# Kernel tuning notes

Measured on AMD Instinct MI355X. Metric: run time of the kernel, lower is better.

## Reference

```python
import jax, jax.numpy as jnp
import numpy as np

B, DIM, N_SIDE = 32, 256, 32
HEADS, DIM_K, DIM_U = 4, 16, 1
DIM_V = 64  # dim_out // heads
EPS = 1e-5

def _rel_pos_idx(n):
    # matches calc_rel_pos: meshgrid(ij) -> (N,2), pairwise diff + (n-1)
    i = np.arange(n)
    pos = np.stack(np.meshgrid(i, i, indexing='ij'), 0).reshape(2, -1).T  # (N, 2)
    rel = pos[None, :] - pos[:, None] + (n - 1)                            # (N, N, 2)
    return rel[..., 0], rel[..., 1]

def _bn(t, gamma, beta):
    # BatchNorm2d in training mode: batch stats over (B, H, W), biased var
    mu = t.mean(axis=(0, 2, 3), keepdims=True)
    var = t.var(axis=(0, 2, 3), keepdims=True)
    xhat = (t - mu) * jax.lax.rsqrt(var + EPS)
    return xhat * gamma[None, :, None, None] + beta[None, :, None, None]

def setup_inputs() -> dict:
    key = jax.random.key(0)
    ks = jax.random.split(key, 5)
    rl = 2 * N_SIDE - 1
    return {
        'x': jax.random.normal(ks[0], (B, DIM, N_SIDE, N_SIDE), jnp.float32),
        'w_q': jax.random.normal(ks[1], (DIM_K * HEADS, DIM), jnp.float32) * 0.05,
        'w_k': jax.random.normal(ks[2], (DIM_K * DIM_U, DIM), jnp.float32) * 0.05,
        'w_v': jax.random.normal(ks[3], (DIM_V * DIM_U, DIM), jnp.float32) * 0.05,
        'gamma_q': jnp.ones((DIM_K * HEADS,), jnp.float32),
        'beta_q': jnp.zeros((DIM_K * HEADS,), jnp.float32),
        'gamma_v': jnp.ones((DIM_V * DIM_U,), jnp.float32),
        'beta_v': jnp.zeros((DIM_V * DIM_U,), jnp.float32),
        'rel_pos_emb': jax.random.normal(ks[4], (rl, rl, DIM_K, DIM_U), jnp.float32),
    }

def reference(x, w_q, w_k, w_v, gamma_q, beta_q, gamma_v, beta_v, rel_pos_emb):
    b, c, hh, ww = x.shape
    n = hh * ww
    # 1x1 convs as channel contractions
    q = _bn(jnp.einsum('oc,bchw->bohw', w_q, x), gamma_q, beta_q)
    k = jnp.einsum('oc,bchw->bohw', w_k, x)
    v = _bn(jnp.einsum('oc,bchw->bohw', w_v, x), gamma_v, beta_v)
    q = q.reshape(b, HEADS, DIM_K, n)   # b h k n
    k = k.reshape(b, DIM_U, DIM_K, n)   # b u k m
    v = v.reshape(b, DIM_U, DIM_V, n)   # b u v m
    k = jax.nn.softmax(k, axis=-1)
    # content lambda
    lam_c = jnp.einsum('bukm,buvm->bkv', k, v)
    Yc = jnp.einsum('bhkn,bkv->bhvn', q, lam_c)
    # positional lambda via relative-position embedding gather
    ni, mi = _rel_pos_idx(N_SIDE)
    emb = rel_pos_emb[ni, mi]                      # (n, n, k, u)
    lam_p = jnp.einsum('nmku,buvm->bnkv', emb, v)  # dominant compute
    Yp = jnp.einsum('bhkn,bnkv->bhvn', q, lam_p)
    Y = Yc + Yp                                    # b h v n
    return Y.reshape(b, HEADS * DIM_V, hh, ww)
```

## Files before the change

kernel.cpp:

```cpp
#include <hip/hip_runtime.h>

using u16 = unsigned short;
using u32 = unsigned int;

typedef __attribute__((ext_vector_type(4))) float f32x4;
typedef __attribute__((ext_vector_type(4))) u16 u16x4;
typedef __attribute__((ext_vector_type(8))) u16 u16x8;
typedef __attribute__((ext_vector_type(8))) short s16x8;

__device__ __forceinline__ u16 f2bf(float f) {
  u32 x = __builtin_bit_cast(u32, f);
  x += 0x7fffu + ((x >> 16) & 1u);
  return (u16)(x >> 16);
}
__device__ __forceinline__ float bf2f(u16 u) {
  u32 x = ((u32)u) << 16;
  return __builtin_bit_cast(float, x);
}

__device__ __forceinline__ void glds16(const u16* gsrc, u16* ldst) {
  __builtin_amdgcn_global_load_lds(
      (const __attribute__((address_space(1))) unsigned int*)gsrc,
      (__attribute__((address_space(3))) unsigned int*)ldst, 16, 0, 0);
}

__global__ __launch_bounds__(256) void k_prep(
    const float* __restrict__ wq, const float* __restrict__ wk,
    const float* __restrict__ wv, const float* __restrict__ R,
    u16* __restrict__ Wb, u16* __restrict__ APre)
{
  const int blk = blockIdx.x;
  const int t = threadIdx.x;
  if (blk < 144) {
    const int o = blk;
    const float* src = (o < 64) ? (wq + o * 256)
                     : (o < 80) ? (wk + (o - 64) * 256)
                                : (wv + (o - 80) * 256);
    Wb[o * 256 + t] = f2bf(src[t]);
  } else {
    const int di = blk - 144;
    const int w = t >> 6, l = t & 63;
    const int g = l >> 4, k = l & 15;
    for (int j1 = w; j1 < 32; j1 += 4) {
      u16x8 o8;
#pragma unroll
      for (int e = 0; e < 8; ++e) {
        int dj = 8 * g + e - j1 + 31;
        o8[e] = f2bf(R[(di * 63 + dj) * 16 + k]);
      }
      *(u16x8*)(APre + ((di * 32 + j1) * 64 + l) * 8) = o8;
    }
  }
}

union ProjSmem {
  u16 XLb[64][264];
  float SS[2][160];
};

__global__ __launch_bounds__(256) void k_proj(
    const float* __restrict__ x, const u16* __restrict__ Wb,
    float* __restrict__ q_raw, float* __restrict__ k_raw,
    float* __restrict__ v_raw,
    float* __restrict__ qs1, float* __restrict__ qs2,
    float* __restrict__ vs1, float* __restrict__ vs2)
{
  __shared__ ProjSmem PS;
  const int b  = blockIdx.x >> 4;
  const int p0 = (blockIdx.x & 15) * 64;
  const int t  = threadIdx.x;

  {
    const int p4 = (t & 15) * 4;
    const int cb = (t >> 4);
#pragma unroll
    for (int i = 0; i < 8; ++i) {
      const int c = 2 * (i * 16 + cb);
      f32x4 xa = *(const f32x4*)&x[(b * 256 + c) * 1024 + p0 + p4];
      f32x4 xb = *(const f32x4*)&x[(b * 256 + c + 1) * 1024 + p0 + p4];
#pragma unroll
      for (int j = 0; j < 4; ++j) {
        u32 pk = (u32)f2bf(xa[j]) | ((u32)f2bf(xb[j]) << 16);
        *(u32*)&PS.XLb[p4 + j][c] = pk;
      }
    }
  }
  __syncthreads();

  const int w  = t >> 6;
  const int l  = t & 63;
  const int g  = l >> 4;
  const int cc = l & 15;
  const int p  = p0 + w * 16 + cc;

  f32x4 acc[9];
  const f32x4 fz = {0.f, 0.f, 0.f, 0.f};
#pragma unroll
  for (int mt = 0; mt < 9; ++mt) acc[mt] = fz;

#pragma unroll
  for (int ko = 0; ko < 8; ++ko) {
    s16x8 bfr = *(const s16x8*)&PS.XLb[w * 16 + cc][ko * 32 + g * 8];
#pragma unroll
    for (int mt = 0; mt < 9; ++mt) {
      s16x8 afr = *(const s16x8*)&Wb[(mt * 16 + cc) * 256 + ko * 32 + g * 8];
      acc[mt] = __builtin_amdgcn_mfma_f32_16x16x32_bf16(afr, bfr, acc[mt], 0, 0, 0);
    }
  }

#pragma unroll
  for (int mt = 0; mt < 9; ++mt) {
#pragma unroll
    for (int r = 0; r < 4; ++r) {
      const int o = mt * 16 + 4 * g + r;
      const float val = acc[mt][r];
      if (mt < 4)       q_raw[(b * 64 + o) * 1024 + p] = val;
      else if (mt == 4) k_raw[(b * 16 + (o - 64)) * 1024 + p] = val;
      else              v_raw[(b * 64 + (o - 80)) * 1024 + p] = val;
    }
  }

  __syncthreads();
  {
    float* ss = &PS.SS[0][0];
    for (int i = t; i < 320; i += 256) ss[i] = 0.f;
  }
  __syncthreads();
#pragma unroll
  for (int mt = 0; mt < 9; ++mt) {
    if (mt == 4) continue;
#pragma unroll
    for (int r = 0; r < 4; ++r) {
      float s1 = acc[mt][r];
      float s2 = s1 * s1;
#pragma unroll
      for (int off = 1; off < 16; off <<= 1) {
        s1 += __shfl_xor(s1, off);
        s2 += __shfl_xor(s2, off);
      }
      if (cc == 0) {
        const int o = mt * 16 + 4 * g + r;
        atomicAdd(&PS.SS[0][o], s1);
        atomicAdd(&PS.SS[1][o], s2);
      }
    }
  }
  __syncthreads();
  if (t < 64) {
    atomicAdd(&qs1[t], PS.SS[0][t]);
    atomicAdd(&qs2[t], PS.SS[1][t]);
  } else if (t >= 80 && t < 144) {
    atomicAdd(&vs1[t - 80], PS.SS[0][t]);
    atomicAdd(&vs2[t - 80], PS.SS[1][t]);
  }
}

__global__ __launch_bounds__(256) void k_soft(
    const float* __restrict__ k_raw,
    float* __restrict__ kmax, float* __restrict__ kinv)
{
  const int t = threadIdx.x;
  const int w = t >> 6, lane = t & 63;
  const int row = blockIdx.x * 4 + w;
  const f32x4* kr4 = (const f32x4*)(k_raw + row * 1024 + lane * 16);
  f32x4 a0 = kr4[0], a1 = kr4[1], a2 = kr4[2], a3 = kr4[3];
  float mx = -3.0e38f;
#pragma unroll
  for (int j = 0; j < 4; ++j)
    mx = fmaxf(mx, fmaxf(fmaxf(a0[j], a1[j]), fmaxf(a2[j], a3[j])));
#pragma unroll
  for (int off = 32; off; off >>= 1) mx = fmaxf(mx, __shfl_xor(mx, off));
  float s = 0.f;
#pragma unroll
  for (int j = 0; j < 4; ++j)
    s += __expf(a0[j] - mx) + __expf(a1[j] - mx)
       + __expf(a2[j] - mx) + __expf(a3[j] - mx);
#pragma unroll
  for (int off = 32; off; off >>= 1) s += __shfl_xor(s, off);
  if (lane == 0) { kmax[row] = mx; kinv[row] = 1.0f / s; }
}

__global__ __launch_bounds__(256) void k_nl(
    const float* __restrict__ v_raw,
    const float* __restrict__ vs1, const float* __restrict__ vs2,
    const float* __restrict__ gv, const float* __restrict__ bv,
    const float* __restrict__ k_raw, const float* __restrict__ kmax,
    const float* __restrict__ kinv,
    u16* __restrict__ vnF, float* __restrict__ lam_c)
{
  __shared__ float VN[64][136];
  __shared__ float KE[16][132];
  const int b  = blockIdx.x >> 3;
  const int m0 = (blockIdx.x & 7) * 128;
  const int t  = threadIdx.x;
  {
    const int v = t & 63, mseg = t >> 6;
    const float invN = 1.0f / 32768.0f;
    const float mu = vs1[v] * invN;
    const float var = vs2[v] * invN - mu * mu;
    const float sc = rsqrtf(var + 1e-5f) * gv[v];
    const float bi = bv[v] - mu * sc;
    const int i2 = (m0 >> 5) + mseg;
    const float* src = v_raw + (b * 64 + v) * 1024 + i2 * 32;
    u16* dstF = vnF + ((b * 32 + i2) * 4 + (v >> 4)) * 512 + (v & 15) * 8;
#pragma unroll
    for (int lg = 0; lg < 4; ++lg) {
      f32x4 a = *(const f32x4*)(src + lg * 8);
      f32x4 c = *(const f32x4*)(src + lg * 8 + 4);
      f32x4 na, nc;
      u16x8 o8;
#pragma unroll
      for (int j = 0; j < 4; ++j) {
        na[j] = a[j] * sc + bi;
        nc[j] = c[j] * sc + bi;
        o8[j] = f2bf(na[j]);
        o8[4 + j] = f2bf(nc[j]);
      }
      *(f32x4*)&VN[v][mseg * 32 + lg * 8] = na;
      *(f32x4*)&VN[v][mseg * 32 + lg * 8 + 4] = nc;
      *(u16x8*)(dstF + lg * 128) = o8;
    }
  }
  {
    const int kc = t >> 4, mm = (t & 15) * 8;
    const int row = b * 16 + kc;
    const float* kr = k_raw + row * 1024 + m0 + mm;
    const float mx = kmax[row], iv = kinv[row];
#pragma unroll
    for (int j = 0; j < 8; ++j) KE[kc][mm + j] = __expf(kr[j] - mx) * iv;
  }
  __syncthreads();
  const int kc = t & 15, vg = t >> 4;
  float acc[4] = {0.f, 0.f, 0.f, 0.f};
  for (int m4 = 0; m4 < 128; m4 += 4) {
    f32x4 ke = *(const f32x4*)&KE[kc][m4];
#pragma unroll
    for (int j = 0; j < 4; ++j) {
      f32x4 vv = *(const f32x4*)&VN[vg * 4 + j][m4];
      acc[j] += ke[0] * vv[0] + ke[1] * vv[1] + ke[2] * vv[2] + ke[3] * vv[3];
    }
  }
#pragma unroll
  for (int j = 0; j < 4; ++j)
    atomicAdd(&lam_c[(b * 16 + kc) * 64 + vg * 4 + j], acc[j]);
}

union KMainSmem {
  struct {
    u16 AL[2][8192];
    u16 BL[2][2][2048];
  } st;
  float YL[2][256][18];
};

__global__ __launch_bounds__(512, 4) void k_main(
    const u16* __restrict__ APre, const u16* __restrict__ vnF,
    const float* __restrict__ q_raw, const float* __restrict__ lam_c,
    const float* __restrict__ qs1, const float* __restrict__ qs2,
    const float* __restrict__ gq, const float* __restrict__ bq,
    float* __restrict__ out)
{
  __shared__ alignas(16) KMainSmem S;
  __shared__ float QL[2][64][17];
  const int bid  = blockIdx.x;
  const int xcd  = bid & 7;
  const int sb   = bid >> 3;
  const int pl   = sb & 1;
  const int rest = sb >> 1;
  const int i1   = rest >> 1;
  const int half = rest & 1;
  const int bBase = xcd * 4 + pl * 2;
  const int t  = threadIdx.x;
  const int w  = t >> 6;
  const int bw = w >> 2;
  const int wl = w & 3;
  const int l  = t & 63;
  const int g  = l >> 4;
  const int c  = l & 15;
  const int b  = bBase + bw;

  const u16* vFw = vnF + b * 65536;

  f32x4 acc[4][4];
  const f32x4 fz = {0.f, 0.f, 0.f, 0.f};
#pragma unroll
  for (int nn = 0; nn < 4; ++nn)
#pragma unroll
    for (int tt = 0; tt < 4; ++tt) acc[nn][tt] = fz;

  auto stage = [&](int p, int nb) {
    const u16* asrc = APre + ((p - i1 + 31) * 32 + half * 16) * 512
                    + w * 1024 + l * 8;
    glds16(asrc, &S.st.AL[nb][w * 1024]);
    glds16(asrc + 512, &S.st.AL[nb][w * 1024 + 512]);
    const u16* bsrc = vFw + p * 2048 + wl * 512 + l * 8;
    glds16(bsrc, &S.st.BL[nb][bw][wl * 512]);
  };

  stage(0, 0);
  {
    const int bw2 = t >> 8;
    const int o = (t & 255) >> 2, ns = (t & 3) * 4;
    const float invN = 1.0f / 32768.0f;
    const float mu = qs1[o] * invN;
    const float var = qs2[o] * invN - mu * mu;
    const float rs = rsqrtf(var + 1e-5f);
    const float sc = rs * gq[o];
    const float bi = bq[o] - mu * sc;
    f32x4 qa = *(const f32x4*)&q_raw[((bBase + bw2) * 64 + o) * 1024
                                     + i1 * 32 + half * 16 + ns];
#pragma unroll
    for (int j = 0; j < 4; ++j) QL[bw2][o][ns + j] = qa[j] * sc + bi;
  }
  __syncthreads();

  for (int p = 0; p < 32; ++p) {
    const int cur = p & 1;
    if (p < 31) stage(p + 1, cur ^ 1);
    __builtin_amdgcn_sched_barrier(0);
    s16x8 afr[4], bfr[4];
#pragma unroll
    for (int nn = 0; nn < 4; ++nn)
      afr[nn] = *(const s16x8*)&S.st.AL[cur][(wl * 4 + nn) * 512 + l * 8];
#pragma unroll
    for (int tt = 0; tt < 4; ++tt)
      bfr[tt] = *(const s16x8*)&S.st.BL[cur][bw][tt * 512 + l * 8];
#pragma unroll
    for (int nn = 0; nn < 4; ++nn)
#pragma unroll
      for (int tt = 0; tt < 4; ++tt)
        acc[nn][tt] = __builtin_amdgcn_mfma_f32_16x16x32_bf16(
            afr[nn], bfr[tt], acc[nn][tt], 0, 0, 0);
    asm volatile("s_waitcnt vmcnt(0)" ::: "memory");
    __builtin_amdgcn_sched_barrier(0);
    __builtin_amdgcn_s_barrier();
    __builtin_amdgcn_sched_barrier(0);
  }

  {
    const float* lcb = lam_c + b * 1024;
#pragma unroll
    for (int tt = 0; tt < 4; ++tt)
#pragma unroll
      for (int r = 0; r < 4; ++r) {
        const float lv = lcb[(4 * g + r) * 64 + tt * 16 + c];
#pragma unroll
        for (int nn = 0; nn < 4; ++nn) acc[nn][tt][r] += lv;
      }
  }
#pragma unroll
  for (int nn = 0; nn < 4; ++nn) {
    const int j1loc = wl * 4 + nn;
#pragma unroll
    for (int h = 0; h < 4; ++h) {
      const float q0 = QL[bw][h * 16 + 4 * g + 0][j1loc];
      const float q1 = QL[bw][h * 16 + 4 * g + 1][j1loc];
      const float q2 = QL[bw][h * 16 + 4 * g + 2][j1loc];
      const float q3 = QL[bw][h * 16 + 4 * g + 3][j1loc];
#pragma unroll
      for (int tt = 0; tt < 4; ++tt) {
        float sY = q0 * acc[nn][tt][0] + q1 * acc[nn][tt][1]
                 + q2 * acc[nn][tt][2] + q3 * acc[nn][tt][3];
        sY += __shfl_xor(sY, 16);
        sY += __shfl_xor(sY, 32);
        if (g == h) S.YL[bw][h * 64 + tt * 16 + c][j1loc] = sY;
      }
    }
  }
  __syncthreads();
#pragma unroll
  for (int it = 0; it < 4; ++it) {
    const int bw2 = t >> 8;
    const int o  = ((t & 255) >> 2) + it * 64;
    const int nf = (t & 3) * 4;
    f32x4 v4 = *(const f32x4*)&S.YL[bw2][o][nf];
    *(f32x4*)&out[((bBase + bw2) * 256 + o) * 1024 + i1 * 32 + half * 16 + nf] = v4;
  }
}

extern "C" void kernel_launch(void* const* d_in, const int* in_sizes, int n_in,
                              void* d_out, int out_size, void* d_ws, size_t ws_size,
                              hipStream_t stream) {
  const float* x  = (const float*)d_in[0];
  const float* wq = (const float*)d_in[1];
  const float* wk = (const float*)d_in[2];
  const float* wv = (const float*)d_in[3];
  const float* gq = (const float*)d_in[4];
  const float* bq = (const float*)d_in[5];
  const float* gv = (const float*)d_in[6];
  const float* bv = (const float*)d_in[7];
  const float* R  = (const float*)d_in[8];
  float* out = (float*)d_out;

  float* wsf   = (float*)d_ws;
  float* q_raw = wsf;
  float* k_raw = q_raw + 32 * 64 * 1024;
  float* v_raw = k_raw + 32 * 16 * 1024;
  float* lam_c = v_raw + 32 * 64 * 1024;
  float* qs1   = lam_c + 32 * 16 * 64;
  float* qs2   = qs1 + 64;
  float* vs1   = qs2 + 64;
  float* vs2   = vs1 + 64;
  float* kmax  = vs2 + 64;
  float* kinv  = kmax + 512;
  u16*   vn    = (u16*)(kinv + 512);
  u16*   vnF   = vn + 32 * 64 * 1024;
  u16*   APre  = vnF + 32 * 65536;
  u16*   Wb    = APre + 63 * 32 * 512;

  hipMemsetAsync(lam_c, 0, (32 * 16 * 64 + 256) * sizeof(float), stream);
  k_prep<<<207, 256, 0, stream>>>(wq, wk, wv, R, Wb, APre);
  k_proj<<<512, 256, 0, stream>>>(x, Wb, q_raw, k_raw, v_raw, qs1, qs2, vs1, vs2);
  k_soft<<<128, 256, 0, stream>>>(k_raw, kmax, kinv);
  k_nl<<<256, 256, 0, stream>>>(v_raw, vs1, vs2, gv, bv, k_raw, kmax, kinv, vnF, lam_c);
  k_main<<<1024, 512, 0, stream>>>(APre, vnF, q_raw, lam_c, qs1, qs2, gq, bq, out);
}
```

Measured before the change: 141.1 us.

## Share B tiles across two query rows in k_main and fuse softmax stats into k_nl

k_main now gives each block one batch and two adjacent query rows instead of two batches and one row. The V tile is loaded once and shared, and the A (embedding) tiles are staged through a three-slot ring because the two row groups need offset diagonals. This cuts global and LDS traffic for B. Separately, the k_soft kernel is removed: each k_nl block recomputes the softmax max and sum for its 16 rows, which saves a launch but repeats that reduction across 8 blocks per batch.

```diff
diff --git a/kernel.cpp b/kernel.cpp
--- a/kernel.cpp
+++ b/kernel.cpp
@@ -155,44 +155,41 @@
   }
 }
 
-__global__ __launch_bounds__(256) void k_soft(
-    const float* __restrict__ k_raw,
-    float* __restrict__ kmax, float* __restrict__ kinv)
-{
-  const int t = threadIdx.x;
-  const int w = t >> 6, lane = t & 63;
-  const int row = blockIdx.x * 4 + w;
-  const f32x4* kr4 = (const f32x4*)(k_raw + row * 1024 + lane * 16);
-  f32x4 a0 = kr4[0], a1 = kr4[1], a2 = kr4[2], a3 = kr4[3];
-  float mx = -3.0e38f;
-#pragma unroll
-  for (int j = 0; j < 4; ++j)
-    mx = fmaxf(mx, fmaxf(fmaxf(a0[j], a1[j]), fmaxf(a2[j], a3[j])));
-#pragma unroll
-  for (int off = 32; off; off >>= 1) mx = fmaxf(mx, __shfl_xor(mx, off));
-  float s = 0.f;
-#pragma unroll
-  for (int j = 0; j < 4; ++j)
-    s += __expf(a0[j] - mx) + __expf(a1[j] - mx)
-       + __expf(a2[j] - mx) + __expf(a3[j] - mx);
-#pragma unroll
-  for (int off = 32; off; off >>= 1) s += __shfl_xor(s, off);
-  if (lane == 0) { kmax[row] = mx; kinv[row] = 1.0f / s; }
-}
-
 __global__ __launch_bounds__(256) void k_nl(
     const float* __restrict__ v_raw,
     const float* __restrict__ vs1, const float* __restrict__ vs2,
     const float* __restrict__ gv, const float* __restrict__ bv,
-    const float* __restrict__ k_raw, const float* __restrict__ kmax,
-    const float* __restrict__ kinv,
+    const float* __restrict__ k_raw,
     u16* __restrict__ vnF, float* __restrict__ lam_c)
 {
   __shared__ float VN[64][136];
   __shared__ float KE[16][132];
+  __shared__ float KMX[16], KIV[16];
   const int b  = blockIdx.x >> 3;
   const int m0 = (blockIdx.x & 7) * 128;
   const int t  = threadIdx.x;
+  const int wv4 = t >> 6, lane = t & 63;
+
+  for (int rr = wv4; rr < 16; rr += 4) {
+    const int row = b * 16 + rr;
+    const f32x4* kr4 = (const f32x4*)(k_raw + row * 1024 + lane * 16);
+    f32x4 a0 = kr4[0], a1 = kr4[1], a2 = kr4[2], a3 = kr4[3];
+    float mx = -3.0e38f;
+#pragma unroll
+    for (int j = 0; j < 4; ++j)
+      mx = fmaxf(mx, fmaxf(fmaxf(a0[j], a1[j]), fmaxf(a2[j], a3[j])));
+#pragma unroll
+    for (int off = 32; off; off >>= 1) mx = fmaxf(mx, __shfl_xor(mx, off));
+    float s = 0.f;
+#pragma unroll
+    for (int j = 0; j < 4; ++j)
+      s += __expf(a0[j] - mx) + __expf(a1[j] - mx)
+         + __expf(a2[j] - mx) + __expf(a3[j] - mx);
+#pragma unroll
+    for (int off = 32; off; off >>= 1) s += __shfl_xor(s, off);
+    if (lane == 0) { KMX[rr] = mx; KIV[rr] = 1.0f / s; }
+  }
+
   {
     const int v = t & 63, mseg = t >> 6;
     const float invN = 1.0f / 32768.0f;
@@ -221,15 +218,17 @@
       *(u16x8*)(dstF + lg * 128) = o8;
     }
   }
+  __syncthreads();
+
   {
     const int kc = t >> 4, mm = (t & 15) * 8;
-    const int row = b * 16 + kc;
-    const float* kr = k_raw + row * 1024 + m0 + mm;
-    const float mx = kmax[row], iv = kinv[row];
+    const float* kr = k_raw + (b * 16 + kc) * 1024 + m0 + mm;
+    const float mx = KMX[kc], iv = KIV[kc];
 #pragma unroll
     for (int j = 0; j < 8; ++j) KE[kc][mm + j] = __expf(kr[j] - mx) * iv;
   }
   __syncthreads();
+
   const int kc = t & 15, vg = t >> 4;
   float acc[4] = {0.f, 0.f, 0.f, 0.f};
   for (int m4 = 0; m4 < 128; m4 += 4) {
@@ -247,8 +246,8 @@
 
 union KMainSmem {
   struct {
-    u16 AL[2][8192];
-    u16 BL[2][2][2048];
+    u16 AS[3][8192];
+    u16 BB[2][2048];
   } st;
   float YL[2][256][18];
 };
@@ -265,21 +264,21 @@
   const int bid  = blockIdx.x;
   const int xcd  = bid & 7;
   const int sb   = bid >> 3;
-  const int pl   = sb & 1;
-  const int rest = sb >> 1;
-  const int i1   = rest >> 1;
+  const int b    = xcd * 4 + (sb & 3);
+  const int rest = sb >> 2;
+  const int i1p  = rest >> 1;
   const int half = rest & 1;
-  const int bBase = xcd * 4 + pl * 2;
-  const int t  = threadIdx.x;
-  const int w  = t >> 6;
-  const int bw = w >> 2;
-  const int wl = w & 3;
-  const int l  = t & 63;
-  const int g  = l >> 4;
-  const int c  = l & 15;
-  const int b  = bBase + bw;
-
-  const u16* vFw = vnF + b * 65536;
+  const int a0   = 2 * i1p;
+  const int h16  = half * 16;
+  const int t   = threadIdx.x;
+  const int w   = t >> 6;
+  const int grp = w >> 2;
+  const int wl  = w & 3;
+  const int l   = t & 63;
+  const int g   = l >> 4;
+  const int c   = l & 15;
+
+  const u16* vF = vnF + b * 65536;
 
   f32x4 acc[4][4];
   const f32x4 fz = {0.f, 0.f, 0.f, 0.f};
@@ -288,43 +287,53 @@
 #pragma unroll
     for (int tt = 0; tt < 4; ++tt) acc[nn][tt] = fz;
 
-  auto stage = [&](int p, int nb) {
-    const u16* asrc = APre + ((p - i1 + 31) * 32 + half * 16) * 512
-                    + w * 1024 + l * 8;
-    glds16(asrc, &S.st.AL[nb][w * 1024]);
-    glds16(asrc + 512, &S.st.AL[nb][w * 1024 + 512]);
-    const u16* bsrc = vFw + p * 2048 + wl * 512 + l * 8;
-    glds16(bsrc, &S.st.BL[nb][bw][wl * 512]);
+  auto stageA = [&](int di, int slot) {
+    const u16* asrc = APre + (di * 32 + h16) * 512 + w * 1024 + l * 8;
+    u16* adst = &S.st.AS[slot][w * 1024];
+    glds16(asrc, adst);
+    glds16(asrc + 512, adst + 512);
   };
-
-  stage(0, 0);
-  {
-    const int bw2 = t >> 8;
-    const int o = (t & 255) >> 2, ns = (t & 3) * 4;
+  auto stageB = [&](int i2, int buf) {
+    if (w < 4) {
+      const u16* bsrc = vF + i2 * 2048 + w * 512 + l * 8;
+      glds16(bsrc, &S.st.BB[buf][w * 512]);
+    }
+  };
+
+  stageA(30 - a0, 0);
+  stageA(31 - a0, 1);
+  stageB(0, 0);
+  {
+    const int g2 = t >> 8;
+    const int o  = (t & 255) >> 2;
+    const int ns = (t & 3) * 4;
     const float invN = 1.0f / 32768.0f;
     const float mu = qs1[o] * invN;
     const float var = qs2[o] * invN - mu * mu;
-    const float rs = rsqrtf(var + 1e-5f);
-    const float sc = rs * gq[o];
+    const float sc = rsqrtf(var + 1e-5f) * gq[o];
     const float bi = bq[o] - mu * sc;
-    f32x4 qa = *(const f32x4*)&q_raw[((bBase + bw2) * 64 + o) * 1024
-                                     + i1 * 32 + half * 16 + ns];
-#pragma unroll
-    for (int j = 0; j < 4; ++j) QL[bw2][o][ns + j] = qa[j] * sc + bi;
-  }
-  __syncthreads();
-
-  for (int p = 0; p < 32; ++p) {
-    const int cur = p & 1;
-    if (p < 31) stage(p + 1, cur ^ 1);
+    f32x4 qa = *(const f32x4*)&q_raw[(b * 64 + o) * 1024
+                                     + (a0 + g2) * 32 + h16 + ns];
+#pragma unroll
+    for (int j = 0; j < 4; ++j) QL[g2][o][ns + j] = qa[j] * sc + bi;
+  }
+  __syncthreads();
+
+  for (int s = 0; s < 32; ++s) {
+    const int bcur = s & 1;
+    if (s < 31) {
+      stageA(32 - a0 + s, (s + 2) % 3);
+      stageB(s + 1, bcur ^ 1);
+    }
     __builtin_amdgcn_sched_barrier(0);
+    const int myslot = (s + 1 - grp) % 3;
     s16x8 afr[4], bfr[4];
 #pragma unroll
     for (int nn = 0; nn < 4; ++nn)
-      afr[nn] = *(const s16x8*)&S.st.AL[cur][(wl * 4 + nn) * 512 + l * 8];
+      afr[nn] = *(const s16x8*)&S.st.AS[myslot][(wl * 4 + nn) * 512 + l * 8];
 #pragma unroll
     for (int tt = 0; tt < 4; ++tt)
-      bfr[tt] = *(const s16x8*)&S.st.BL[cur][bw][tt * 512 + l * 8];
+      bfr[tt] = *(const s16x8*)&S.st.BB[bcur][tt * 512 + l * 8];
 #pragma unroll
     for (int nn = 0; nn < 4; ++nn)
 #pragma unroll
@@ -353,28 +362,28 @@
     const int j1loc = wl * 4 + nn;
 #pragma unroll
     for (int h = 0; h < 4; ++h) {
-      const float q0 = QL[bw][h * 16 + 4 * g + 0][j1loc];
-      const float q1 = QL[bw][h * 16 + 4 * g + 1][j1loc];
-      const float q2 = QL[bw][h * 16 + 4 * g + 2][j1loc];
-      const float q3 = QL[bw][h * 16 + 4 * g + 3][j1loc];
+      const float q0 = QL[grp][h * 16 + 4 * g + 0][j1loc];
+      const float q1 = QL[grp][h * 16 + 4 * g + 1][j1loc];
+      const float q2 = QL[grp][h * 16 + 4 * g + 2][j1loc];
+      const float q3 = QL[grp][h * 16 + 4 * g + 3][j1loc];
 #pragma unroll
       for (int tt = 0; tt < 4; ++tt) {
         float sY = q0 * acc[nn][tt][0] + q1 * acc[nn][tt][1]
                  + q2 * acc[nn][tt][2] + q3 * acc[nn][tt][3];
         sY += __shfl_xor(sY, 16);
         sY += __shfl_xor(sY, 32);
-        if (g == h) S.YL[bw][h * 64 + tt * 16 + c][j1loc] = sY;
+        if (g == h) S.YL[grp][h * 64 + tt * 16 + c][j1loc] = sY;
       }
     }
   }
   __syncthreads();
 #pragma unroll
   for (int it = 0; it < 4; ++it) {
-    const int bw2 = t >> 8;
+    const int g2 = t >> 8;
     const int o  = ((t & 255) >> 2) + it * 64;
     const int nf = (t & 3) * 4;
-    f32x4 v4 = *(const f32x4*)&S.YL[bw2][o][nf];
-    *(f32x4*)&out[((bBase + bw2) * 256 + o) * 1024 + i1 * 32 + half * 16 + nf] = v4;
+    f32x4 v4 = *(const f32x4*)&S.YL[g2][o][nf];
+    *(f32x4*)&out[(b * 256 + o) * 1024 + (a0 + g2) * 32 + h16 + nf] = v4;
   }
 }
 
@@ -411,7 +420,6 @@
   hipMemsetAsync(lam_c, 0, (32 * 16 * 64 + 256) * sizeof(float), stream);
   k_prep<<<207, 256, 0, stream>>>(wq, wk, wv, R, Wb, APre);
   k_proj<<<512, 256, 0, stream>>>(x, Wb, q_raw, k_raw, v_raw, qs1, qs2, vs1, vs2);
-  k_soft<<<128, 256, 0, stream>>>(k_raw, kmax, kinv);
-  k_nl<<<256, 256, 0, stream>>>(v_raw, vs1, vs2, gv, bv, k_raw, kmax, kinv, vnF, lam_c);
+  k_nl<<<256, 256, 0, stream>>>(v_raw, vs1, vs2, gv, bv, k_raw, vnF, lam_c);
   k_main<<<1024, 512, 0, stream>>>(APre, vnF, q_raw, lam_c, qs1, qs2, gq, bq, out);
 }
```

Measured after the change: 141.3 us. No clear change (+0.1%).
